# Performance work log

Measured on AMD Instinct MI355X. Metric: run time of the kernel, lower is better.

## Reference

```python
import jax, jax.numpy as jnp
import numpy as np

STAGES = 3
CAUSAL = True


def sine_positional_encoding(T, D, dtype=jnp.float32):
    # keras_nlp SinePositionEncoding: interleaved sin/cos, base 10000
    pos = jnp.arange(T, dtype=dtype)[:, None]            # [T,1]
    i = jnp.arange(D)[None, :]                            # [1,D]
    angle = pos / jnp.power(jnp.asarray(10000.0, dtype), (2 * (i // 2)).astype(dtype) / D)
    return jnp.where(i % 2 == 0, jnp.sin(angle), jnp.cos(angle))  # [T,D]


def setup_inputs() -> dict:
    key = jax.random.key(0)
    kX, kWp, kbp, kWf, kbf = jax.random.split(key, 5)
    B, T, D = 4, 4096, 1024
    X = jax.random.normal(kX, (B, T, D), dtype=jnp.float32)
    # data_projection: D -> (stages+1)*D
    Wp = jax.random.normal(kWp, (D, (STAGES + 1) * D), dtype=jnp.float32) / np.sqrt(D)
    bp = jnp.zeros(((STAGES + 1) * D,), dtype=jnp.float32)
    # filters: D -> stages*D (applied to positional encoding)
    Wf = jax.random.normal(kWf, (D, STAGES * D), dtype=jnp.float32) / np.sqrt(D)
    bf = jnp.zeros((STAGES * D,), dtype=jnp.float32)
    return {"X": X, "Wp": Wp, "bp": bp, "Wf": Wf, "bf": bf}


def reference(X, Wp, bp, Wf, bf):
    B, T, D = X.shape
    # linear projections of data: [B,T,stages+1,D]
    xp = (jnp.einsum('btd,de->bte', X, Wp) + bp).reshape(B, T, STAGES + 1, D)
    # filters from sinusoidal positional encoding (batch-independent): [T,stages,D]
    pos = sine_positional_encoding(T, D, X.dtype)
    f = (pos @ Wf + bf).reshape(T, STAGES, D)
    if CAUSAL:
        # zero-pad time axis to 2T -> circular FFT conv becomes linear (causal) conv
        xp = jnp.concatenate([xp, jnp.zeros_like(xp)], axis=1)   # [B,2T,S+1,D]
        f = jnp.concatenate([f, jnp.zeros_like(f)], axis=0)      # [2T,S,D]
    L = xp.shape[1]
    F = jnp.fft.rfft(f, axis=0)                                   # [L//2+1,S,D]
    y = xp[:, :, 0, :]                                            # [B,L,D]
    for i in range(STAGES):
        conv = jnp.fft.irfft(jnp.fft.rfft(y, axis=1) * F[None, :, i, :], n=L, axis=1)
        y = conv * xp[:, :, i + 1, :]
    return y[:, :T, :] if CAUSAL else y
```

## Files before the change

kernel.cpp:

```cpp
#include <hip/hip_runtime.h>
#include <math.h>

#define T_LEN 4096
#define D_DIM 1024
#define B_DIM 4
#define N_STAGES 3
#define FT 512

typedef unsigned short bf16_t;
typedef __bf16 bf16x8 __attribute__((ext_vector_type(8)));
typedef float f32x4 __attribute__((ext_vector_type(4)));

#define SW(i) ((i) ^ ((((unsigned)(i)) >> 4) & 15))

__device__ __forceinline__ bf16_t f2bf(float f) {
    union { float f; unsigned u; } v; v.f = f;
    unsigned r = v.u + 0x7FFFu + ((v.u >> 16) & 1u);
    return (bf16_t)(r >> 16);
}
__device__ __forceinline__ float bf2f(bf16_t h) {
    union { unsigned u; float f; } v; v.u = ((unsigned)h) << 16;
    return v.f;
}
__device__ __forceinline__ float2 cmul(float2 a, float2 b) {
    return make_float2(a.x * b.x - a.y * b.y, a.x * b.y + a.y * b.x);
}
__device__ __forceinline__ float2 cadd(float2 a, float2 b) { return make_float2(a.x + b.x, a.y + b.y); }
__device__ __forceinline__ float2 csub(float2 a, float2 b) { return make_float2(a.x - b.x, a.y - b.y); }
__device__ __forceinline__ float2 conjf2(float2 a) { return make_float2(a.x, -a.y); }

#define GLOAD_LDS16(gp, lp) __builtin_amdgcn_global_load_lds( \
    (const __attribute__((address_space(1))) void*)(gp),      \
    (__attribute__((address_space(3))) void*)(lp), 16, 0, 0)

__global__ __launch_bounds__(256) void pos_kernel(bf16_t* __restrict__ posbf) {
    int idx = blockIdx.x * 256 + threadIdx.x;
    int t = idx >> 10;
    int k = idx & 1023;
    float e = (float)(k & ~1) / (float)D_DIM;
    float r = exp2f(-e * 13.287712379549449f);
    float angle = (float)t * r;
    float v = (k & 1) ? cosf(angle) : sinf(angle);
    posbf[idx] = f2bf(v);
}

__global__ __launch_bounds__(256) void f32_to_bf16_kernel(const float* __restrict__ in,
                                                          bf16_t* __restrict__ out, int n8) {
    int i = blockIdx.x * 256 + threadIdx.x;
    if (i >= n8) return;
    float4 a = ((const float4*)in)[i * 2];
    float4 b = ((const float4*)in)[i * 2 + 1];
    ((ushort4*)out)[i * 2]     = make_ushort4(f2bf(a.x), f2bf(a.y), f2bf(a.z), f2bf(a.w));
    ((ushort4*)out)[i * 2 + 1] = make_ushort4(f2bf(b.x), f2bf(b.y), f2bf(b.z), f2bf(b.w));
}

__global__ __launch_bounds__(256) void transpose_to_bf16(const float* __restrict__ in,
                                                         bf16_t* __restrict__ out, int K, int N) {
    __shared__ float tile[32][33];
    const int n0 = blockIdx.x * 32;
    const int k0 = blockIdx.y * 32;
    const int tx = threadIdx.x & 31;
    const int ty = threadIdx.x >> 5;
    for (int i = ty; i < 32; i += 8)
        tile[i][tx] = in[(size_t)(k0 + i) * N + n0 + tx];
    __syncthreads();
    for (int i = ty; i < 32; i += 8)
        out[(size_t)(n0 + i) * K + k0 + tx] = f2bf(tile[tx][i]);
}

template <int MODE>
__global__ __launch_bounds__(256) void mfma_gemm(const bf16_t* __restrict__ A,
                                                 const bf16_t* __restrict__ BT,
                                                 const float* __restrict__ bias,
                                                 void* __restrict__ outv,
                                                 int M, int N, int K, int nbx) {
    constexpr int SMEM_BYTES = (MODE == 0) ? (128 * 136 * 2) : (128 * 132 * 4);
    __shared__ __align__(16) char smem[SMEM_BYTES];
    bf16_t* As = (bf16_t*)smem;
    bf16_t* Bs = (bf16_t*)(smem + 8192);

    const int tid = threadIdx.x;
    const int lane = tid & 63;
    const int w = tid >> 6;
    const int wr = w >> 1, wc = w & 1;

    const int nwg = gridDim.x;
    const int q = nwg >> 3;
    const int swz = (blockIdx.x & 7) * q + (blockIdx.x >> 3);
    const int by = swz / nbx, bx = swz - by * nbx;
    const int row0 = by * 128, col0 = bx * 128;

    f32x4 acc[4][4];
#pragma unroll
    for (int m = 0; m < 4; ++m)
#pragma unroll
        for (int n = 0; n < 4; ++n) acc[m][n] = (f32x4)(0.0f);

    int offs[2], rr[2], kk8[2];
#pragma unroll
    for (int c = 0; c < 2; ++c) {
        offs[c] = (w * 2 + c) * 1024 + lane * 16;
        rr[c] = offs[c] >> 6;
        kk8[c] = ((offs[c] >> 4) & 3) * 8;
    }

    for (int k0 = 0; k0 < K; k0 += 32) {
#pragma unroll
        for (int c = 0; c < 2; ++c) {
            const bf16_t* gA = A + (size_t)(row0 + rr[c]) * K + k0 + kk8[c];
            GLOAD_LDS16(gA, As + (w * 2 + c) * 512);
            const bf16_t* gB = BT + (size_t)(col0 + rr[c]) * K + k0 + kk8[c];
            GLOAD_LDS16(gB, Bs + (w * 2 + c) * 512);
        }
        __syncthreads();

        bf16x8 af[4], bfr[4];
#pragma unroll
        for (int m = 0; m < 4; ++m)
            af[m] = *(const bf16x8*)&As[(wr * 64 + m * 16 + (lane & 15)) * 32 + (lane >> 4) * 8];
#pragma unroll
        for (int n = 0; n < 4; ++n)
            bfr[n] = *(const bf16x8*)&Bs[(wc * 64 + n * 16 + (lane & 15)) * 32 + (lane >> 4) * 8];
#pragma unroll
        for (int m = 0; m < 4; ++m)
#pragma unroll
            for (int n = 0; n < 4; ++n)
                acc[m][n] = __builtin_amdgcn_mfma_f32_16x16x32_bf16(af[m], bfr[n], acc[m][n], 0, 0, 0);
        __syncthreads();
    }

    if (MODE == 0) {
        bf16_t* Cs = (bf16_t*)smem;
#pragma unroll
        for (int m = 0; m < 4; ++m)
#pragma unroll
            for (int n = 0; n < 4; ++n) {
                int cl = wc * 64 + n * 16 + (lane & 15);
                int rlb = wr * 64 + m * 16 + ((lane >> 4) << 2);
                float bb = bias[col0 + cl];
#pragma unroll
                for (int j = 0; j < 4; ++j)
                    Cs[cl * 136 + rlb + j] = f2bf(acc[m][n][j] + bb);
            }
        __syncthreads();
        int dl = tid >> 1, th = tid & 1;
        int cc = col0 + dl;
        int s = cc >> 10, d = cc & 1023;
        int b = row0 >> 12;
        int t0 = (row0 & 4095) + th * 64;
        uint4* dst = (uint4*)&((bf16_t*)outv)[((size_t)(s * 4 + b) * 1024 + d) * 4096 + t0];
        const uint4* src = (const uint4*)&Cs[dl * 136 + th * 64];
#pragma unroll
        for (int j = 0; j < 8; ++j) dst[j] = src[j];
    } else {
        float* CsF = (float*)smem;
#pragma unroll
        for (int m = 0; m < 4; ++m)
#pragma unroll
            for (int n = 0; n < 4; ++n) {
                int cl = wc * 64 + n * 16 + (lane & 15);
                int rlb = wr * 64 + m * 16 + ((lane >> 4) << 2);
                float bb = bias[col0 + cl];
#pragma unroll
                for (int j = 0; j < 4; ++j)
                    CsF[cl * 132 + rlb + j] = acc[m][n][j] + bb;
            }
        __syncthreads();
        int dl = tid >> 1, th = tid & 1;
        int cc = col0 + dl;
        uint4* dst = (uint4*)&((float*)outv)[(size_t)cc * 4096 + row0 + th * 64];
        const uint4* src = (const uint4*)&CsF[dl * 132 + th * 64];
#pragma unroll
        for (int j = 0; j < 16; ++j) dst[j] = src[j];
    }
}

template <int INV>
__device__ __forceinline__ void bfly4(float2& a, float2& b, float2& c, float2& d) {
    float2 t0 = cadd(a, c), t1 = csub(a, c), t2 = cadd(b, d), t3 = csub(b, d);
    float2 it3 = INV ? make_float2(-t3.y, t3.x) : make_float2(t3.y, -t3.x);
    a = cadd(t0, t2); b = cadd(t1, it3); c = csub(t0, t2); d = csub(t1, it3);
}

template <int INV>
__device__ __forceinline__ void dft8(float2 (&x)[8]) {
    bfly4<INV>(x[0], x[2], x[4], x[6]);
    bfly4<INV>(x[1], x[3], x[5], x[7]);
    const float s2 = 0.70710678118654752f;
    const float2 o1 = INV ? make_float2(s2, s2) : make_float2(s2, -s2);
    const float2 o3 = INV ? make_float2(-s2, s2) : make_float2(-s2, -s2);
    x[3] = cmul(x[3], o1);
    x[5] = INV ? make_float2(-x[5].y, x[5].x) : make_float2(x[5].y, -x[5].x);
    x[7] = cmul(x[7], o3);
    float2 F0 = cadd(x[0], x[1]), F4 = csub(x[0], x[1]);
    float2 F1 = cadd(x[2], x[3]), F5 = csub(x[2], x[3]);
    float2 F2 = cadd(x[4], x[5]), F6 = csub(x[4], x[5]);
    float2 F3 = cadd(x[6], x[7]), F7 = csub(x[6], x[7]);
    x[0] = F0; x[1] = F1; x[2] = F2; x[3] = F3;
    x[4] = F4; x[5] = F5; x[6] = F6; x[7] = F7;
}

template <int INV, int M>
__device__ __forceinline__ void r8_pass(float2* __restrict__ s, const float2* __restrict__ Wu) {
    const int p = threadIdx.x;
    const int r = p & (M - 1);
    const int jm = p - r;
    float2 x[8];
#pragma unroll
    for (int c = 0; c < 8; ++c) x[c] = s[SW(p + 512 * c)];
    __syncthreads();
    dft8<INV>(x);
    const int base = 8 * jm + r;
    if (M == 512) {
#pragma unroll
        for (int q = 0; q < 8; ++q) s[SW(base + q * 512)] = x[q];
    } else {
        float2 w1 = Wu[2 * jm];
        if (INV) w1.y = -w1.y;
        float2 w2 = cmul(w1, w1);
        float2 w3 = cmul(w2, w1);
        float2 w4 = cmul(w2, w2);
        s[SW(base)]         = x[0];
        s[SW(base + M)]     = cmul(w1, x[1]);
        s[SW(base + 2 * M)] = cmul(w2, x[2]);
        s[SW(base + 3 * M)] = cmul(w3, x[3]);
        s[SW(base + 4 * M)] = cmul(w4, x[4]);
        s[SW(base + 5 * M)] = cmul(cmul(w4, w1), x[5]);
        s[SW(base + 6 * M)] = cmul(cmul(w4, w2), x[6]);
        s[SW(base + 7 * M)] = cmul(cmul(w4, w3), x[7]);
    }
    __syncthreads();
}

template <int INV>
__device__ __forceinline__ void fft4096_ip(float2* __restrict__ s, const float2* __restrict__ Wu) {
    r8_pass<INV, 1>(s, Wu);
    r8_pass<INV, 8>(s, Wu);
    r8_pass<INV, 64>(s, Wu);
    r8_pass<INV, 512>(s, Wu);
}

template <int INV, int M>
__device__ __forceinline__ void r8_pass4s(float2 (*__restrict__ s)[4096],
                                          const float2* __restrict__ Wu) {
    const int p = threadIdx.x;
    const int r = p & (M - 1);
    const int jm = p - r;
    const int base = 8 * jm + r;
    float2 w1, w2, w3, w4, w5, w6, w7;
    if (M != 512) {
        w1 = Wu[2 * jm];
        if (INV) w1.y = -w1.y;
        w2 = cmul(w1, w1); w3 = cmul(w2, w1); w4 = cmul(w2, w2);
        w5 = cmul(w4, w1); w6 = cmul(w4, w2); w7 = cmul(w4, w3);
    }
    {
        float2 x[2][8];
#pragma unroll
        for (int e = 0; e < 2; ++e)
#pragma unroll
            for (int c = 0; c < 8; ++c) x[e][c] = s[e][SW(p + 512 * c)];
        __syncthreads();
#pragma unroll
        for (int e = 0; e < 2; ++e) {
            dft8<INV>(x[e]);
            if (M == 512) {
#pragma unroll
                for (int q = 0; q < 8; ++q) s[e][SW(base + q * 512)] = x[e][q];
            } else {
                s[e][SW(base)]         = x[e][0];
                s[e][SW(base + M)]     = cmul(w1, x[e][1]);
                s[e][SW(base + 2 * M)] = cmul(w2, x[e][2]);
                s[e][SW(base + 3 * M)] = cmul(w3, x[e][3]);
                s[e][SW(base + 4 * M)] = cmul(w4, x[e][4]);
                s[e][SW(base + 5 * M)] = cmul(w5, x[e][5]);
                s[e][SW(base + 6 * M)] = cmul(w6, x[e][6]);
                s[e][SW(base + 7 * M)] = cmul(w7, x[e][7]);
            }
        }
    }
    {
        float2 y[2][8];
#pragma unroll
        for (int e = 0; e < 2; ++e)
#pragma unroll
            for (int c = 0; c < 8; ++c) y[e][c] = s[2 + e][SW(p + 512 * c)];
        __syncthreads();
#pragma unroll
        for (int e = 0; e < 2; ++e) {
            dft8<INV>(y[e]);
            if (M == 512) {
#pragma unroll
                for (int q = 0; q < 8; ++q) s[2 + e][SW(base + q * 512)] = y[e][q];
            } else {
                s[2 + e][SW(base)]         = y[e][0];
                s[2 + e][SW(base + M)]     = cmul(w1, y[e][1]);
                s[2 + e][SW(base + 2 * M)] = cmul(w2, y[e][2]);
                s[2 + e][SW(base + 3 * M)] = cmul(w3, y[e][3]);
                s[2 + e][SW(base + 4 * M)] = cmul(w4, y[e][4]);
                s[2 + e][SW(base + 5 * M)] = cmul(w5, y[e][5]);
                s[2 + e][SW(base + 6 * M)] = cmul(w6, y[e][6]);
                s[2 + e][SW(base + 7 * M)] = cmul(w7, y[e][7]);
            }
        }
    }
}

template <int INV>
__device__ __forceinline__ void fft4096_ip4s(float2 (*__restrict__ s)[4096],
                                             const float2* __restrict__ Wu) {
    r8_pass4s<INV, 1>(s, Wu);
    r8_pass4s<INV, 8>(s, Wu);
    r8_pass4s<INV, 64>(s, Wu);
    r8_pass4s<INV, 512>(s, Wu);
    __syncthreads();
}

__device__ __forceinline__ void init_wu(float2* __restrict__ Wu) {
    const int tid = threadIdx.x;
#pragma unroll
    for (int u = 0; u < 4; ++u) {
        int k = u * FT + tid;
        float sn, cs;
        __sincosf((float)k * -7.669903939428206e-4f, &sn, &cs);
        Wu[k] = make_float2(cs, sn);
    }
}

__device__ __forceinline__ float2 spec_load(const void* spec, int bf, size_t row, int k) {
    if (bf) {
        ushort2 h = ((const ushort2*)spec)[row * 4097 + k];
        return make_float2(bf2f(h.x), bf2f(h.y));
    }
    return ((const float2*)spec)[row * 4097 + k];
}
__device__ __forceinline__ void spec_store(void* spec, int bf, size_t row, int k, float2 v) {
    if (bf) ((ushort2*)spec)[row * 4097 + k] = make_ushort2(f2bf(v.x), f2bf(v.y));
    else    ((float2*)spec)[row * 4097 + k] = v;
}

__global__ __launch_bounds__(FT)
void filter_fft_kernel(const float* __restrict__ fT,
                       void* __restrict__ specv,
                       int spec_bf16) {
    __shared__ __align__(16) float2 sA[4096];
    __shared__ __align__(16) float2 Wu[2048];
    const int tid = threadIdx.x;
    const size_t row = blockIdx.x;
    init_wu(Wu);
    const float4* f4 = (const float4*)&fT[row * T_LEN];
#pragma unroll
    for (int u = 0; u < 2; ++u) {
        int j = u * FT + tid;
        float4 v = f4[j];
        sA[SW(2 * j)]     = make_float2(v.x, v.y);
        sA[SW(2 * j + 1)] = make_float2(v.z, v.w);
    }
#pragma unroll
    for (int u = 0; u < 4; ++u) {
        int n = 2048 + u * FT + tid;
        sA[SW(n)] = make_float2(0.0f, 0.0f);
    }
    __syncthreads();
    fft4096_ip<0>(sA, Wu);
#pragma unroll
    for (int u = 0; u < 4; ++u) {
        int s = u * FT + tid;
        if (s < 2047) {
            int k = s + 1, nk = 4096 - k;
            float2 Zk = sA[SW(k)], Zn = sA[SW(nk)];
            float2 Ye = make_float2(0.5f * (Zk.x + Zn.x), 0.5f * (Zk.y - Zn.y));
            float2 Yo = make_float2(0.5f * (Zk.y + Zn.y), -0.5f * (Zk.x - Zn.x));
            float2 w = Wu[k];
            float2 wYo = cmul(w, Yo);
            spec_store(specv, spec_bf16, row, k, cadd(Ye, wYo));
            spec_store(specv, spec_bf16, row, nk, conjf2(csub(Ye, wYo)));
        }
    }
    if (tid == 0) {
        float2 Z0 = sA[SW(0)];
        spec_store(specv, spec_bf16, row, 0,    make_float2(Z0.x + Z0.y, 0.0f));
        spec_store(specv, spec_bf16, row, 4096, make_float2(Z0.x - Z0.y, 0.0f));
        spec_store(specv, spec_bf16, row, 2048, conjf2(sA[SW(2048)]));
    }
}

__global__ __launch_bounds__(FT)
void conv_kernel(const bf16_t* __restrict__ xpT,
                 const void* __restrict__ specv,
                 int spec_bf16,
                 bf16_t* __restrict__ yT) {
    __shared__ __align__(16) float2 sA[4][4096];
    __shared__ __align__(16) float2 Wu[2048];
    const int tid = threadIdx.x;
    const int d = blockIdx.x;
    init_wu(Wu);

#pragma unroll
    for (int bb = 0; bb < 4; ++bb) {
        const ushort4* y4 = (const ushort4*)&xpT[((size_t)bb * 1024 + d) * T_LEN];
#pragma unroll
        for (int u = 0; u < 2; ++u) {
            int j = u * FT + tid;
            ushort4 h = y4[j];
            sA[bb][SW(2 * j)]     = make_float2(bf2f(h.x), bf2f(h.y));
            sA[bb][SW(2 * j + 1)] = make_float2(bf2f(h.z), bf2f(h.w));
        }
#pragma unroll
        for (int u = 0; u < 4; ++u) {
            int n = 2048 + u * FT + tid;
            sA[bb][SW(n)] = make_float2(0.0f, 0.0f);
        }
    }
    __syncthreads();

    const float scale = 1.0f / 4096.0f;
    for (int st = 0; st < N_STAGES; ++st) {
        fft4096_ip4s<0>(sA, Wu);
        const size_t row = (size_t)st * 1024 + d;
#pragma unroll
        for (int u = 0; u < 4; ++u) {
            int s = u * FT + tid;
            if (s < 2047) {
                int k = s + 1, nk = 4096 - k;
                float2 w = Wu[k];
                float2 cw = conjf2(w);
                float2 Fk = spec_load(specv, spec_bf16, row, k);
                float2 Fn = spec_load(specv, spec_bf16, row, nk);
#pragma unroll
                for (int bb = 0; bb < 4; ++bb) {
                    float2 Zk = sA[bb][SW(k)], Zn = sA[bb][SW(nk)];
                    float2 Ye = make_float2(0.5f * (Zk.x + Zn.x), 0.5f * (Zk.y - Zn.y));
                    float2 Yo = make_float2(0.5f * (Zk.y + Zn.y), -0.5f * (Zk.x - Zn.x));
                    float2 wYo = cmul(w, Yo);
                    float2 Yk = cadd(Ye, wYo);
                    float2 Ynk = conjf2(csub(Ye, wYo));
                    float2 Hk = cmul(Yk, Fk);
                    float2 Hn = cmul(Ynk, Fn);
                    float2 He = make_float2(0.5f * (Hk.x + Hn.x), 0.5f * (Hk.y - Hn.y));
                    float2 Hd = make_float2(0.5f * (Hk.x - Hn.x), 0.5f * (Hk.y + Hn.y));
                    float2 Ho = cmul(cw, Hd);
                    sA[bb][SW(k)]  = make_float2(He.x - Ho.y, He.y + Ho.x);
                    sA[bb][SW(nk)] = make_float2(He.x + Ho.y, Ho.x - He.y);
                }
            }
        }
        if (tid == 0) {
            float2 F0 = spec_load(specv, spec_bf16, row, 0);
            float2 FN = spec_load(specv, spec_bf16, row, 4096);
            float2 F2 = spec_load(specv, spec_bf16, row, 2048);
#pragma unroll
            for (int bb = 0; bb < 4; ++bb) {
                float2 Z0 = sA[bb][SW(0)];
                float Y0 = Z0.x + Z0.y, YN = Z0.x - Z0.y;
                float2 H0 = make_float2(Y0 * F0.x, Y0 * F0.y);
                float2 HN = make_float2(YN * FN.x, YN * FN.y);
                float2 He0 = make_float2(0.5f * (H0.x + HN.x), 0.5f * (H0.y + HN.y));
                float2 Ho0 = make_float2(0.5f * (H0.x - HN.x), 0.5f * (H0.y - HN.y));
                sA[bb][SW(0)] = make_float2(He0.x - Ho0.y, He0.y + Ho0.x);
                float2 H2 = cmul(conjf2(sA[bb][SW(2048)]), F2);
                sA[bb][SW(2048)] = conjf2(H2);
            }
        }
        __syncthreads();
        fft4096_ip4s<1>(sA, Wu);

        if (st < N_STAGES - 1) {
#pragma unroll
            for (int bb = 0; bb < 4; ++bb) {
                const ushort4* g4 = (const ushort4*)&xpT[((size_t)((st + 1) * 4 + bb) * 1024 + d) * T_LEN];
#pragma unroll
                for (int u = 0; u < 2; ++u) {
                    int j = u * FT + tid;
                    ushort4 h = g4[j];
                    float2 v0 = sA[bb][SW(2 * j)], v1 = sA[bb][SW(2 * j + 1)];
                    sA[bb][SW(2 * j)]     = make_float2(v0.x * scale * bf2f(h.x), v0.y * scale * bf2f(h.y));
                    sA[bb][SW(2 * j + 1)] = make_float2(v1.x * scale * bf2f(h.z), v1.y * scale * bf2f(h.w));
                }
#pragma unroll
                for (int u = 0; u < 4; ++u) {
                    int n = 2048 + u * FT + tid;
                    sA[bb][SW(n)] = make_float2(0.0f, 0.0f);
                }
            }
            __syncthreads();
        } else {
#pragma unroll
            for (int bb = 0; bb < 4; ++bb) {
                const ushort4* g4 = (const ushort4*)&xpT[((size_t)((st + 1) * 4 + bb) * 1024 + d) * T_LEN];
                ushort4* yrow = (ushort4*)&yT[((size_t)bb * 1024 + d) * T_LEN];
#pragma unroll
                for (int u = 0; u < 2; ++u) {
                    int j = u * FT + tid;
                    ushort4 h = g4[j];
                    float2 v0 = sA[bb][SW(2 * j)], v1 = sA[bb][SW(2 * j + 1)];
                    yrow[j] = make_ushort4(f2bf(v0.x * scale * bf2f(h.x)),
                                           f2bf(v0.y * scale * bf2f(h.y)),
                                           f2bf(v1.x * scale * bf2f(h.z)),
                                           f2bf(v1.y * scale * bf2f(h.w)));
                }
            }
        }
    }
}

__global__ __launch_bounds__(256) void transpose_out(const bf16_t* __restrict__ yT,
                                                     float* __restrict__ out) {
    __shared__ float tile[32][33];
    const int tb = blockIdx.z;
    const int t0 = blockIdx.x * 32;
    const int d0 = blockIdx.y * 32;
    const int tx = threadIdx.x & 31;
    const int ty = threadIdx.x >> 5;
    for (int i = ty; i < 32; i += 8)
        tile[i][tx] = bf2f(yT[((size_t)tb * 1024 + d0 + i) * 4096 + t0 + tx]);
    __syncthreads();
    for (int i = ty; i < 32; i += 8)
        out[((size_t)tb * 4096 + t0 + i) * 1024 + d0 + tx] = tile[tx][i];
}

extern "C" void kernel_launch(void* const* d_in, const int* in_sizes, int n_in,
                              void* d_out, int out_size, void* d_ws, size_t ws_size,
                              hipStream_t stream) {
    const float* X   = (const float*)d_in[0];
    const float* Wp  = (const float*)d_in[1];
    const float* bp  = (const float*)d_in[2];
    const float* Wf  = (const float*)d_in[3];
    const float* bfv = (const float*)d_in[4];
    float* out = (float*)d_out;
    char* ws = (char*)d_ws;

    const size_t XPT_BYTES  = (size_t)134217728;
    const size_t SPEC_F32_B = (size_t)3 * 1024 * 4097 * 8;
    const size_t SPEC_BF_B  = (size_t)3 * 1024 * 4097 * 4;
    const size_t XBF_BYTES  = (size_t)33554432;
    const size_t WPT_BYTES  = (size_t)8388608;

    bf16_t* xpT   = (bf16_t*)ws;
    bf16_t* posbf = (bf16_t*)ws;
    bf16_t* WfT   = (bf16_t*)(ws + 16777216);
    float*  fT    = (float*)(ws + 33554432);
    void*   spec  = (void*)(ws + XPT_BYTES);

    int spec_bf16;
    size_t spec_bytes;
    if (ws_size >= XPT_BYTES + SPEC_F32_B + XBF_BYTES + WPT_BYTES) {
        spec_bf16 = 0; spec_bytes = SPEC_F32_B;
    } else {
        spec_bf16 = 1; spec_bytes = SPEC_BF_B;
    }
    bf16_t* Xbf = (bf16_t*)(ws + XPT_BYTES + spec_bytes);
    bf16_t* WpT = (bf16_t*)(ws + XPT_BYTES + spec_bytes + XBF_BYTES);
    bf16_t* yT  = Xbf;

    pos_kernel<<<(T_LEN * D_DIM) / 256, 256, 0, stream>>>(posbf);

    transpose_to_bf16<<<dim3(3072 / 32, 1024 / 32), 256, 0, stream>>>(Wf, WfT, 1024, 3072);
    mfma_gemm<1><<<768, 256, 0, stream>>>(posbf, WfT, bfv, fT, 4096, 3072, 1024, 24);

    filter_fft_kernel<<<N_STAGES * D_DIM, FT, 0, stream>>>(fT, spec, spec_bf16);

    f32_to_bf16_kernel<<<8192, 256, 0, stream>>>(X, Xbf, 2097152);
    transpose_to_bf16<<<dim3(4096 / 32, 1024 / 32), 256, 0, stream>>>(Wp, WpT, 1024, 4096);
    mfma_gemm<0><<<4096, 256, 0, stream>>>(Xbf, WpT, bp, xpT, 16384, 4096, 1024, 32);

    conv_kernel<<<D_DIM, FT, 0, stream>>>(xpT, spec, spec_bf16, yT);

    transpose_out<<<dim3(4096 / 32, 1024 / 32, B_DIM), 256, 0, stream>>>(yT, out);
}
```

Measured before the change: 667.7 us.

## Split conv kernel across batch pairs and halve twiddle table in LDS

The conv kernel now launches two blocks per channel, each handling two batch rows instead of four, which halves the LDS signal buffer. The twiddle table is cut from 2048 to 1024 entries, and the upper half is derived by rotating by -pi/4. Together these reduce LDS per block from about 144KB to about 72KB, so two blocks can fit per CU and there are twice as many blocks. The cost is that filter spectrum loads and twiddle setup are duplicated across the pair of blocks, and the untangle step does a little extra arithmetic.

```diff
diff --git a/kernel.cpp b/kernel.cpp
--- a/kernel.cpp
+++ b/kernel.cpp
@@ -28,6 +28,8 @@
 __device__ __forceinline__ float2 cadd(float2 a, float2 b) { return make_float2(a.x + b.x, a.y + b.y); }
 __device__ __forceinline__ float2 csub(float2 a, float2 b) { return make_float2(a.x - b.x, a.y - b.y); }
 __device__ __forceinline__ float2 conjf2(float2 a) { return make_float2(a.x, -a.y); }
+
+#define W8R 0.70710678118654752f
 
 #define GLOAD_LDS16(gp, lp) __builtin_amdgcn_global_load_lds( \
     (const __attribute__((address_space(1))) void*)(gp),      \
@@ -200,6 +202,12 @@
     x[4] = F4; x[5] = F5; x[6] = F6; x[7] = F7;
 }
 
+__device__ __forceinline__ float2 untangle_w(const float2* __restrict__ Wu, int k) {
+    if (k < 1024) return Wu[k];
+    float2 b = Wu[k - 1024];
+    return make_float2(W8R * (b.x + b.y), W8R * (b.y - b.x));
+}
+
 template <int INV, int M>
 __device__ __forceinline__ void r8_pass(float2* __restrict__ s, const float2* __restrict__ Wu) {
     const int p = threadIdx.x;
@@ -241,7 +249,7 @@
 }
 
 template <int INV, int M>
-__device__ __forceinline__ void r8_pass4s(float2 (*__restrict__ s)[4096],
+__device__ __forceinline__ void r8_pass2s(float2 (*__restrict__ s)[4096],
                                           const float2* __restrict__ Wu) {
     const int p = threadIdx.x;
     const int r = p & (M - 1);
@@ -254,76 +262,51 @@
         w2 = cmul(w1, w1); w3 = cmul(w2, w1); w4 = cmul(w2, w2);
         w5 = cmul(w4, w1); w6 = cmul(w4, w2); w7 = cmul(w4, w3);
     }
-    {
-        float2 x[2][8];
-#pragma unroll
-        for (int e = 0; e < 2; ++e)
-#pragma unroll
-            for (int c = 0; c < 8; ++c) x[e][c] = s[e][SW(p + 512 * c)];
-        __syncthreads();
-#pragma unroll
-        for (int e = 0; e < 2; ++e) {
-            dft8<INV>(x[e]);
-            if (M == 512) {
-#pragma unroll
-                for (int q = 0; q < 8; ++q) s[e][SW(base + q * 512)] = x[e][q];
-            } else {
-                s[e][SW(base)]         = x[e][0];
-                s[e][SW(base + M)]     = cmul(w1, x[e][1]);
-                s[e][SW(base + 2 * M)] = cmul(w2, x[e][2]);
-                s[e][SW(base + 3 * M)] = cmul(w3, x[e][3]);
-                s[e][SW(base + 4 * M)] = cmul(w4, x[e][4]);
-                s[e][SW(base + 5 * M)] = cmul(w5, x[e][5]);
-                s[e][SW(base + 6 * M)] = cmul(w6, x[e][6]);
-                s[e][SW(base + 7 * M)] = cmul(w7, x[e][7]);
-            }
-        }
-    }
-    {
-        float2 y[2][8];
-#pragma unroll
-        for (int e = 0; e < 2; ++e)
-#pragma unroll
-            for (int c = 0; c < 8; ++c) y[e][c] = s[2 + e][SW(p + 512 * c)];
-        __syncthreads();
-#pragma unroll
-        for (int e = 0; e < 2; ++e) {
-            dft8<INV>(y[e]);
-            if (M == 512) {
-#pragma unroll
-                for (int q = 0; q < 8; ++q) s[2 + e][SW(base + q * 512)] = y[e][q];
-            } else {
-                s[2 + e][SW(base)]         = y[e][0];
-                s[2 + e][SW(base + M)]     = cmul(w1, y[e][1]);
-                s[2 + e][SW(base + 2 * M)] = cmul(w2, y[e][2]);
-                s[2 + e][SW(base + 3 * M)] = cmul(w3, y[e][3]);
-                s[2 + e][SW(base + 4 * M)] = cmul(w4, y[e][4]);
-                s[2 + e][SW(base + 5 * M)] = cmul(w5, y[e][5]);
-                s[2 + e][SW(base + 6 * M)] = cmul(w6, y[e][6]);
-                s[2 + e][SW(base + 7 * M)] = cmul(w7, y[e][7]);
-            }
-        }
-    }
+    float2 x[2][8];
+#pragma unroll
+    for (int e = 0; e < 2; ++e)
+#pragma unroll
+        for (int c = 0; c < 8; ++c) x[e][c] = s[e][SW(p + 512 * c)];
+    __syncthreads();
+#pragma unroll
+    for (int e = 0; e < 2; ++e) {
+        dft8<INV>(x[e]);
+        if (M == 512) {
+#pragma unroll
+            for (int q = 0; q < 8; ++q) s[e][SW(base + q * 512)] = x[e][q];
+        } else {
+            s[e][SW(base)]         = x[e][0];
+            s[e][SW(base + M)]     = cmul(w1, x[e][1]);
+            s[e][SW(base + 2 * M)] = cmul(w2, x[e][2]);
+            s[e][SW(base + 3 * M)] = cmul(w3, x[e][3]);
+            s[e][SW(base + 4 * M)] = cmul(w4, x[e][4]);
+            s[e][SW(base + 5 * M)] = cmul(w5, x[e][5]);
+            s[e][SW(base + 6 * M)] = cmul(w6, x[e][6]);
+            s[e][SW(base + 7 * M)] = cmul(w7, x[e][7]);
+        }
+    }
+    __syncthreads();
 }
 
 template <int INV>
-__device__ __forceinline__ void fft4096_ip4s(float2 (*__restrict__ s)[4096],
+__device__ __forceinline__ void fft4096_ip2s(float2 (*__restrict__ s)[4096],
                                              const float2* __restrict__ Wu) {
-    r8_pass4s<INV, 1>(s, Wu);
-    r8_pass4s<INV, 8>(s, Wu);
-    r8_pass4s<INV, 64>(s, Wu);
-    r8_pass4s<INV, 512>(s, Wu);
-    __syncthreads();
+    r8_pass2s<INV, 1>(s, Wu);
+    r8_pass2s<INV, 8>(s, Wu);
+    r8_pass2s<INV, 64>(s, Wu);
+    r8_pass2s<INV, 512>(s, Wu);
 }
 
 __device__ __forceinline__ void init_wu(float2* __restrict__ Wu) {
     const int tid = threadIdx.x;
 #pragma unroll
-    for (int u = 0; u < 4; ++u) {
+    for (int u = 0; u < 2; ++u) {
         int k = u * FT + tid;
-        float sn, cs;
-        __sincosf((float)k * -7.669903939428206e-4f, &sn, &cs);
-        Wu[k] = make_float2(cs, sn);
+        if (k < 1024) {
+            float sn, cs;
+            __sincosf((float)k * -7.669903939428206e-4f, &sn, &cs);
+            Wu[k] = make_float2(cs, sn);
+        }
     }
 }
 
@@ -344,7 +327,7 @@
                        void* __restrict__ specv,
                        int spec_bf16) {
     __shared__ __align__(16) float2 sA[4096];
-    __shared__ __align__(16) float2 Wu[2048];
+    __shared__ __align__(16) float2 Wu[1024];
     const int tid = threadIdx.x;
     const size_t row = blockIdx.x;
     init_wu(Wu);
@@ -371,7 +354,7 @@
             float2 Zk = sA[SW(k)], Zn = sA[SW(nk)];
             float2 Ye = make_float2(0.5f * (Zk.x + Zn.x), 0.5f * (Zk.y - Zn.y));
             float2 Yo = make_float2(0.5f * (Zk.y + Zn.y), -0.5f * (Zk.x - Zn.x));
-            float2 w = Wu[k];
+            float2 w = untangle_w(Wu, k);
             float2 wYo = cmul(w, Yo);
             spec_store(specv, spec_bf16, row, k, cadd(Ye, wYo));
             spec_store(specv, spec_bf16, row, nk, conjf2(csub(Ye, wYo)));
@@ -390,46 +373,48 @@
                  const void* __restrict__ specv,
                  int spec_bf16,
                  bf16_t* __restrict__ yT) {
-    __shared__ __align__(16) float2 sA[4][4096];
-    __shared__ __align__(16) float2 Wu[2048];
+    __shared__ __align__(16) float2 sA[2][4096];
+    __shared__ __align__(16) float2 Wu[1024];
     const int tid = threadIdx.x;
-    const int d = blockIdx.x;
+    const int d  = blockIdx.x >> 1;
+    const int pr = blockIdx.x & 1;
     init_wu(Wu);
 
 #pragma unroll
-    for (int bb = 0; bb < 4; ++bb) {
+    for (int e = 0; e < 2; ++e) {
+        const int bb = 2 * pr + e;
         const ushort4* y4 = (const ushort4*)&xpT[((size_t)bb * 1024 + d) * T_LEN];
 #pragma unroll
         for (int u = 0; u < 2; ++u) {
             int j = u * FT + tid;
             ushort4 h = y4[j];
-            sA[bb][SW(2 * j)]     = make_float2(bf2f(h.x), bf2f(h.y));
-            sA[bb][SW(2 * j + 1)] = make_float2(bf2f(h.z), bf2f(h.w));
+            sA[e][SW(2 * j)]     = make_float2(bf2f(h.x), bf2f(h.y));
+            sA[e][SW(2 * j + 1)] = make_float2(bf2f(h.z), bf2f(h.w));
         }
 #pragma unroll
         for (int u = 0; u < 4; ++u) {
             int n = 2048 + u * FT + tid;
-            sA[bb][SW(n)] = make_float2(0.0f, 0.0f);
+            sA[e][SW(n)] = make_float2(0.0f, 0.0f);
         }
     }
     __syncthreads();
 
     const float scale = 1.0f / 4096.0f;
     for (int st = 0; st < N_STAGES; ++st) {
-        fft4096_ip4s<0>(sA, Wu);
+        fft4096_ip2s<0>(sA, Wu);
         const size_t row = (size_t)st * 1024 + d;
 #pragma unroll
         for (int u = 0; u < 4; ++u) {
             int s = u * FT + tid;
             if (s < 2047) {
                 int k = s + 1, nk = 4096 - k;
-                float2 w = Wu[k];
+                float2 w = untangle_w(Wu, k);
                 float2 cw = conjf2(w);
                 float2 Fk = spec_load(specv, spec_bf16, row, k);
                 float2 Fn = spec_load(specv, spec_bf16, row, nk);
 #pragma unroll
-                for (int bb = 0; bb < 4; ++bb) {
-                    float2 Zk = sA[bb][SW(k)], Zn = sA[bb][SW(nk)];
+                for (int e = 0; e < 2; ++e) {
+                    float2 Zk = sA[e][SW(k)], Zn = sA[e][SW(nk)];
                     float2 Ye = make_float2(0.5f * (Zk.x + Zn.x), 0.5f * (Zk.y - Zn.y));
                     float2 Yo = make_float2(0.5f * (Zk.y + Zn.y), -0.5f * (Zk.x - Zn.x));
                     float2 wYo = cmul(w, Yo);
@@ -440,8 +425,8 @@
                     float2 He = make_float2(0.5f * (Hk.x + Hn.x), 0.5f * (Hk.y - Hn.y));
                     float2 Hd = make_float2(0.5f * (Hk.x - Hn.x), 0.5f * (Hk.y + Hn.y));
                     float2 Ho = cmul(cw, Hd);
-                    sA[bb][SW(k)]  = make_float2(He.x - Ho.y, He.y + Ho.x);
-                    sA[bb][SW(nk)] = make_float2(He.x + Ho.y, Ho.x - He.y);
+                    sA[e][SW(k)]  = make_float2(He.x - Ho.y, He.y + Ho.x);
+                    sA[e][SW(nk)] = make_float2(He.x + Ho.y, Ho.x - He.y);
                 }
             }
         }
@@ -450,50 +435,52 @@
             float2 FN = spec_load(specv, spec_bf16, row, 4096);
             float2 F2 = spec_load(specv, spec_bf16, row, 2048);
 #pragma unroll
-            for (int bb = 0; bb < 4; ++bb) {
-                float2 Z0 = sA[bb][SW(0)];
+            for (int e = 0; e < 2; ++e) {
+                float2 Z0 = sA[e][SW(0)];
                 float Y0 = Z0.x + Z0.y, YN = Z0.x - Z0.y;
                 float2 H0 = make_float2(Y0 * F0.x, Y0 * F0.y);
                 float2 HN = make_float2(YN * FN.x, YN * FN.y);
                 float2 He0 = make_float2(0.5f * (H0.x + HN.x), 0.5f * (H0.y + HN.y));
                 float2 Ho0 = make_float2(0.5f * (H0.x - HN.x), 0.5f * (H0.y - HN.y));
-                sA[bb][SW(0)] = make_float2(He0.x - Ho0.y, He0.y + Ho0.x);
-                float2 H2 = cmul(conjf2(sA[bb][SW(2048)]), F2);
-                sA[bb][SW(2048)] = conjf2(H2);
+                sA[e][SW(0)] = make_float2(He0.x - Ho0.y, He0.y + Ho0.x);
+                float2 H2 = cmul(conjf2(sA[e][SW(2048)]), F2);
+                sA[e][SW(2048)] = conjf2(H2);
             }
         }
         __syncthreads();
-        fft4096_ip4s<1>(sA, Wu);
+        fft4096_ip2s<1>(sA, Wu);
 
         if (st < N_STAGES - 1) {
 #pragma unroll
-            for (int bb = 0; bb < 4; ++bb) {
+            for (int e = 0; e < 2; ++e) {
+                const int bb = 2 * pr + e;
                 const ushort4* g4 = (const ushort4*)&xpT[((size_t)((st + 1) * 4 + bb) * 1024 + d) * T_LEN];
 #pragma unroll
                 for (int u = 0; u < 2; ++u) {
                     int j = u * FT + tid;
                     ushort4 h = g4[j];
-                    float2 v0 = sA[bb][SW(2 * j)], v1 = sA[bb][SW(2 * j + 1)];
-                    sA[bb][SW(2 * j)]     = make_float2(v0.x * scale * bf2f(h.x), v0.y * scale * bf2f(h.y));
-                    sA[bb][SW(2 * j + 1)] = make_float2(v1.x * scale * bf2f(h.z), v1.y * scale * bf2f(h.w));
+                    float2 v0 = sA[e][SW(2 * j)], v1 = sA[e][SW(2 * j + 1)];
+                    sA[e][SW(2 * j)]     = make_float2(v0.x * scale * bf2f(h.x), v0.y * scale * bf2f(h.y));
+                    sA[e][SW(2 * j + 1)] = make_float2(v1.x * scale * bf2f(h.z), v1.y * scale * bf2f(h.w));
                 }
 #pragma unroll
                 for (int u = 0; u < 4; ++u) {
                     int n = 2048 + u * FT + tid;
-                    sA[bb][SW(n)] = make_float2(0.0f, 0.0f);
+                    sA[e][SW(n)] = make_float2(0.0f, 0.0f);
                 }
             }
             __syncthreads();
         } else {
 #pragma unroll
-            for (int bb = 0; bb < 4; ++bb) {
+            for (int e = 0; e < 2; ++e) {
+                const int bb = 2 * pr + e;
                 const ushort4* g4 = (const ushort4*)&xpT[((size_t)((st + 1) * 4 + bb) * 1024 + d) * T_LEN];
                 ushort4* yrow = (ushort4*)&yT[((size_t)bb * 1024 + d) * T_LEN];
 #pragma unroll
                 for (int u = 0; u < 2; ++u) {
                     int j = u * FT + tid;
                     ushort4 h = g4[j];
-                    float2 v0 = sA[bb][SW(2 * j)], v1 = sA[bb][SW(2 * j + 1)];
+                    float2 v0 = sA[e][SW(2 * j)], v1 = sA[e][SW(2 * j + 1)];
                     yrow[j] = make_ushort4(f2bf(v0.x * scale * bf2f(h.x)),
                                            f2bf(v0.y * scale * bf2f(h.y)),
                                            f2bf(v1.x * scale * bf2f(h.z)),
@@ -564,7 +551,7 @@
     transpose_to_bf16<<<dim3(4096 / 32, 1024 / 32), 256, 0, stream>>>(Wp, WpT, 1024, 4096);
     mfma_gemm<0><<<4096, 256, 0, stream>>>(Xbf, WpT, bp, xpT, 16384, 4096, 1024, 32);
 
-    conv_kernel<<<D_DIM, FT, 0, stream>>>(xpT, spec, spec_bf16, yT);
+    conv_kernel<<<2 * D_DIM, FT, 0, stream>>>(xpT, spec, spec_bf16, yT);
 
     transpose_out<<<dim3(4096 / 32, 1024 / 32, B_DIM), 256, 0, stream>>>(yT, out);
 }
```

After: 688.8 us. 3.2% more time.
